# Kernel tuning notes

Hardware: AMD Instinct MI355X
Metric: run time of the kernel (lower is better)

Reference implementation:

```python
import jax, jax.numpy as jnp
import numpy as np

B, S, E = 2, 2048, 1024
H = 16
D = E // H  # 64
SCALE = D ** -0.5


def setup_inputs() -> dict:
    key = jax.random.key(0)
    ks = jax.random.split(key, 9)
    w = lambda k: jax.random.normal(k, (E, E), dtype=jnp.float32) * 0.02
    b = lambda k: jax.random.normal(k, (E,), dtype=jnp.float32) * 0.02
    return {
        "hidden_states": jax.random.normal(ks[0], (B, S, E), dtype=jnp.float32),
        "q_w": w(ks[1]), "q_b": b(ks[2]),
        "k_w": w(ks[3]), "k_b": b(ks[4]),
        "v_w": w(ks[5]), "v_b": b(ks[6]),
        "o_w": w(ks[7]), "o_b": b(ks[8]),
    }


def reference(hidden_states, q_w, q_b, k_w, k_b, v_w, v_b, o_w, o_b):
    dtype = hidden_states.dtype
    # torch Linear: y = x @ W^T + b
    q = hidden_states @ q_w.T + q_b
    k = hidden_states @ k_w.T + k_b
    v = hidden_states @ v_w.T + v_b
    # [B,S,E] -> [B*H, S, D]
    split = lambda t: t.reshape(B, S, H, D).transpose(0, 2, 1, 3).reshape(B * H, S, D)
    q, k, v = split(q), split(k), split(v)
    # upcast_attention: fp32 QK^T, scaled (baddbmm with beta=0, no mask)
    scores = SCALE * jnp.einsum("bqd,bkd->bqk", q.astype(jnp.float32), k.astype(jnp.float32))
    # upcast_softmax: fp32 softmax over last dim (transpose_qk=False), cast back
    probs = jax.nn.softmax(scores, axis=-1).astype(dtype)
    # PV bmm, merge heads, out_proj (dropout p=0.0 -> identity)
    out = jnp.einsum("bqk,bkd->bqd", probs, v)
    out = out.reshape(B, H, S, D).transpose(0, 2, 1, 3).reshape(B, S, E)
    return out @ o_w.T + o_b
```

## Files before the change

### kernel.cpp

```cpp
#include <hip/hip_runtime.h>

typedef __bf16 bf16x8 __attribute__((ext_vector_type(8)));
typedef __bf16 bf16x4 __attribute__((ext_vector_type(4)));
typedef float  f32x4  __attribute__((ext_vector_type(4)));

#define CS 0.18033688011112042f

__device__ __forceinline__ float fast_exp2(float x) {
    return __builtin_amdgcn_exp2f(x);
}

__device__ __forceinline__ f32x4 MFMA(bf16x8 a, bf16x8 b, f32x4 c) {
    return __builtin_amdgcn_mfma_f32_16x16x32_bf16(a, b, c, 0, 0, 0);
}

__global__ __launch_bounds__(256) void cvt5_kernel(
    const float* __restrict__ s0, const float* __restrict__ s1,
    const float* __restrict__ s2, const float* __restrict__ s3,
    const float* __restrict__ s4,
    __bf16* __restrict__ d0, __bf16* __restrict__ d1, __bf16* __restrict__ d2,
    __bf16* __restrict__ d3, __bf16* __restrict__ d4)
{
    int blk = blockIdx.x;
    const float* src; __bf16* dst; int base;
    if (blk < 4096)      { src = s0; dst = d0; base = blk; }
    else if (blk < 5120) { src = s1; dst = d1; base = blk - 4096; }
    else if (blk < 6144) { src = s2; dst = d2; base = blk - 5120; }
    else if (blk < 7168) { src = s3; dst = d3; base = blk - 6144; }
    else                 { src = s4; dst = d4; base = blk - 7168; }
    int i = base * 1024 + threadIdx.x * 4;
    float4 v = *(const float4*)(src + i);
    bf16x4 o;
    o[0] = (__bf16)v.x; o[1] = (__bf16)v.y; o[2] = (__bf16)v.z; o[3] = (__bf16)v.w;
    *(bf16x4*)(dst + i) = o;
}

template <typename OutT, int BN>
__device__ __forceinline__ void gemm_core(const __bf16* __restrict__ A,
                                          const __bf16* __restrict__ W,
                                          const float* __restrict__ bias,
                                          OutT* __restrict__ C,
                                          int m0, int n0, bool vtrans)
{
    constexpr int NJ = BN / 32;
    __shared__ __bf16 As[128 * 64];
    __shared__ __bf16 Bs[BN * 64];

    const int tid  = threadIdx.x;
    const int lane = tid & 63;
    const int w    = tid >> 6;
    const int wm   = w & 1;
    const int wn   = w >> 1;
    const int s    = lane & 15;
    const int q    = lane >> 4;

    f32x4 acc[4][NJ];
#pragma unroll
    for (int i = 0; i < 4; i++)
#pragma unroll
        for (int j = 0; j < NJ; j++)
#pragma unroll
            for (int r = 0; r < 4; r++) acc[i][j][r] = 0.0f;

    bf16x8 apre[4], bpre[NJ];
#pragma unroll
    for (int t = 0; t < 4; t++) {
        int c = tid + 256 * t, row = c >> 3, cc = c & 7;
        apre[t] = *(const bf16x8*)(A + (size_t)(m0 + row) * 1024 + cc * 8);
    }
#pragma unroll
    for (int t = 0; t < NJ; t++) {
        int c = tid + 256 * t, row = c >> 3, cc = c & 7;
        bpre[t] = *(const bf16x8*)(W + (size_t)(n0 + row) * 1024 + cc * 8);
    }

    for (int k0 = 0; k0 < 1024; k0 += 64) {
        __syncthreads();
#pragma unroll
        for (int t = 0; t < 4; t++) {
            int c = tid + 256 * t, row = c >> 3, cc = c & 7;
            *(bf16x8*)&As[row * 64 + ((cc ^ (row & 7)) << 3)] = apre[t];
        }
#pragma unroll
        for (int t = 0; t < NJ; t++) {
            int c = tid + 256 * t, row = c >> 3, cc = c & 7;
            *(bf16x8*)&Bs[row * 64 + ((cc ^ (row & 7)) << 3)] = bpre[t];
        }
        __syncthreads();

        if (k0 < 1024 - 64) {
            int kn = k0 + 64;
#pragma unroll
            for (int t = 0; t < 4; t++) {
                int c = tid + 256 * t, row = c >> 3, cc = c & 7;
                apre[t] = *(const bf16x8*)(A + (size_t)(m0 + row) * 1024 + kn + cc * 8);
            }
#pragma unroll
            for (int t = 0; t < NJ; t++) {
                int c = tid + 256 * t, row = c >> 3, cc = c & 7;
                bpre[t] = *(const bf16x8*)(W + (size_t)(n0 + row) * 1024 + kn + cc * 8);
            }
        }

#pragma unroll
        for (int kk = 0; kk < 2; kk++) {
            bf16x8 af[4], bf[NJ];
#pragma unroll
            for (int i = 0; i < 4; i++) {
                int row = wm * 64 + i * 16 + s;
                int idx = row * 64 + ((((kk << 2) + q) ^ (row & 7)) << 3);
                af[i] = *(const bf16x8*)&As[idx];
            }
#pragma unroll
            for (int j = 0; j < NJ; j++) {
                int row = wn * (BN / 2) + j * 16 + s;
                int idx = row * 64 + ((((kk << 2) + q) ^ (row & 7)) << 3);
                bf[j] = *(const bf16x8*)&Bs[idx];
            }
#pragma unroll
            for (int i = 0; i < 4; i++)
#pragma unroll
                for (int j = 0; j < NJ; j++)
                    acc[i][j] = MFMA(af[i], bf[j], acc[i][j]);
        }
    }

    if (vtrans) {
        __bf16* Vt = (__bf16*)C;
#pragma unroll
        for (int j = 0; j < NJ; j++) {
            int col = n0 + wn * (BN / 2) + j * 16 + s;
            int h   = col >> 6;
            int d   = col & 63;
            float bv = bias[col];
#pragma unroll
            for (int i = 0; i < 4; i++) {
                int rowb = m0 + wm * 64 + i * 16 + q * 4;
                int b    = rowb >> 11;
                int srow = rowb & 2047;
                bf16x4 pk;
#pragma unroll
                for (int r = 0; r < 4; r++) pk[r] = (__bf16)(acc[i][j][r] + bv);
                *(bf16x4*)&Vt[(size_t)((b * 16 + h) * 64 + d) * 2048 + srow] = pk;
            }
        }
    } else {
#pragma unroll
        for (int j = 0; j < NJ; j++) {
            int col = n0 + wn * (BN / 2) + j * 16 + s;
            float bv = bias[col];
#pragma unroll
            for (int i = 0; i < 4; i++) {
                int rowb = m0 + wm * 64 + i * 16 + q * 4;
#pragma unroll
                for (int r = 0; r < 4; r++) {
                    C[(size_t)(rowb + r) * 1024 + col] = (OutT)(acc[i][j][r] + bv);
                }
            }
        }
    }
}

__global__ __launch_bounds__(256) void gemm_qkv_kernel(
    const __bf16* __restrict__ X,
    const __bf16* __restrict__ Wq, const float* __restrict__ bq,
    const __bf16* __restrict__ Wk, const float* __restrict__ bk,
    const __bf16* __restrict__ Wv, const float* __restrict__ bv,
    __bf16* __restrict__ Q, __bf16* __restrict__ K, __bf16* __restrict__ Vt)
{
    int mt   = blockIdx.x & 31;
    int ntot = blockIdx.x >> 5;
    int which = ntot >> 3;
    const __bf16* W    = (which == 0) ? Wq : (which == 1) ? Wk : Wv;
    const float*  bias = (which == 0) ? bq : (which == 1) ? bk : bv;
    __bf16*       Out  = (which == 0) ? Q  : (which == 1) ? K  : Vt;
    gemm_core<__bf16, 128>(X, W, bias, Out, mt * 128, (ntot & 7) * 128, which == 2);
}

__global__ __launch_bounds__(256) void gemm_o_kernel(
    const __bf16* __restrict__ Ain, const __bf16* __restrict__ Wo,
    const float* __restrict__ bo, float* __restrict__ Out)
{
    int mt = blockIdx.x & 31;
    int nt = blockIdx.x >> 5;
    gemm_core<float, 64>(Ain, Wo, bo, Out, mt * 128, nt * 64, false);
}

__global__ __launch_bounds__(256, 2) void attn_kernel(
    const __bf16* __restrict__ Q, const __bf16* __restrict__ K,
    const __bf16* __restrict__ Vt, __bf16* __restrict__ O)
{
    __shared__ __bf16 k_lds[128 * 64];
    __shared__ __bf16 vt_lds[64 * 128];
    __shared__ __bf16 p_lds[4 * 32 * 128];

    const int bh = blockIdx.x >> 4;
    const int qt = blockIdx.x & 15;
    const int b  = bh >> 4;
    const int h  = bh & 15;

    const int tid  = threadIdx.x;
    const int lane = tid & 63;
    const int w    = tid >> 6;
    const int s    = lane & 15;
    const int q    = lane >> 4;

    bf16x8 aq[2][2];
#pragma unroll
    for (int i = 0; i < 2; i++)
#pragma unroll
        for (int kd = 0; kd < 2; kd++) {
            int row = qt * 128 + w * 32 + i * 16 + s;
            aq[i][kd] = *(const bf16x8*)(Q + (size_t)(b * 2048 + row) * 1024 +
                                         h * 64 + kd * 32 + q * 8);
        }

    f32x4 acc_o[2][4];
    float lst[2][4];
#pragma unroll
    for (int i = 0; i < 2; i++)
#pragma unroll
        for (int r = 0; r < 4; r++) {
            lst[i][r] = 0.0f;
#pragma unroll
            for (int jd = 0; jd < 4; jd++) acc_o[i][jd][r] = 0.0f;
        }

    const int pbase = w * 32 * 128;

    bf16x8 kpre[4], vpre[4];
#pragma unroll
    for (int t = 0; t < 4; t++) {
        int c = tid + 256 * t;
        int krow = c >> 3, cc = c & 7;
        kpre[t] = *(const bf16x8*)(K + (size_t)(b * 2048 + krow) * 1024 +
                                   h * 64 + cc * 8);
        int d = c >> 4, ck = c & 15;
        vpre[t] = *(const bf16x8*)(Vt + (size_t)(bh * 64 + d) * 2048 + ck * 8);
    }

    for (int kc = 0; kc < 16; kc++) {
        __syncthreads();
#pragma unroll
        for (int t = 0; t < 4; t++) {
            int c = tid + 256 * t;
            int krow = c >> 3, cc = c & 7;
            int rho  = ((krow & 7) << 4) | (krow >> 3);
            *(bf16x8*)&k_lds[rho * 64 + ((cc ^ (rho & 7)) << 3)] = kpre[t];
            int d = c >> 4, ck = c & 15;
            *(bf16x8*)&vt_lds[(d * 16 + (ck ^ (d & 7))) << 3] = vpre[t];
        }
        __syncthreads();

        int kb2 = ((kc + 1) & 15) * 128;
#pragma unroll
        for (int t = 0; t < 4; t++) {
            int c = tid + 256 * t;
            int krow = c >> 3, cc = c & 7;
            kpre[t] = *(const bf16x8*)(K + (size_t)(b * 2048 + kb2 + krow) * 1024 +
                                       h * 64 + cc * 8);
            int d = c >> 4, ck = c & 15;
            vpre[t] = *(const bf16x8*)(Vt + (size_t)(bh * 64 + d) * 2048 + kb2 + ck * 8);
        }

        f32x4 sc[2][8];
#pragma unroll
        for (int i = 0; i < 2; i++)
#pragma unroll
            for (int j = 0; j < 8; j++)
#pragma unroll
                for (int r = 0; r < 4; r++) sc[i][j][r] = 0.0f;
#pragma unroll
        for (int kd = 0; kd < 2; kd++) {
#pragma unroll
            for (int j = 0; j < 8; j++) {
                int row = j * 16 + s;
                int idx = row * 64 + ((((kd << 2) + q) ^ (row & 7)) << 3);
                bf16x8 bf = *(const bf16x8*)&k_lds[idx];
                sc[0][j] = MFMA(aq[0][kd], bf, sc[0][j]);
                sc[1][j] = MFMA(aq[1][kd], bf, sc[1][j]);
            }
        }

#pragma unroll
        for (int i = 0; i < 2; i++)
#pragma unroll
            for (int r = 0; r < 4; r++) {
                int prow = i * 16 + q * 4 + r;
                bf16x8 pk;
                float rsum = 0.0f;
#pragma unroll
                for (int j = 0; j < 8; j++) {
                    float p = fast_exp2(sc[i][j][r] * CS);
                    rsum += p;
                    pk[j] = (__bf16)p;
                }
                lst[i][r] += rsum;
                int chunkp = s ^ (prow & 15);
                *(bf16x8*)&p_lds[pbase + prow * 128 + (chunkp << 3)] = pk;
            }

#pragma unroll
        for (int kk = 0; kk < 4; kk++) {
            bf16x8 ap[2];
#pragma unroll
            for (int i = 0; i < 2; i++) {
                int prow = i * 16 + s;
                int chunkr = ((kk << 2) + q) ^ s;
                ap[i] = *(const bf16x8*)&p_lds[pbase + prow * 128 + (chunkr << 3)];
            }
#pragma unroll
            for (int jd = 0; jd < 4; jd++) {
                int d    = jd * 16 + s;
                int vidx = (d * 16 + (((kk << 2) + q) ^ (d & 7))) << 3;
                bf16x8 bv = *(const bf16x8*)&vt_lds[vidx];
                acc_o[0][jd] = MFMA(ap[0], bv, acc_o[0][jd]);
                acc_o[1][jd] = MFMA(ap[1], bv, acc_o[1][jd]);
            }
        }
    }

#pragma unroll
    for (int i = 0; i < 2; i++)
#pragma unroll
        for (int r = 0; r < 4; r++) {
#pragma unroll
            for (int off = 1; off < 16; off <<= 1)
                lst[i][r] += __shfl_xor(lst[i][r], off);
        }

#pragma unroll
    for (int i = 0; i < 2; i++)
#pragma unroll
        for (int jd = 0; jd < 4; jd++)
#pragma unroll
            for (int r = 0; r < 4; r++) {
                int row = qt * 128 + w * 32 + i * 16 + q * 4 + r;
                int col = h * 64 + jd * 16 + s;
                float v = acc_o[i][jd][r] / lst[i][r];
                O[(size_t)(b * 2048 + row) * 1024 + col] = (__bf16)v;
            }
}

extern "C" void kernel_launch(void* const* d_in, const int* in_sizes, int n_in,
                              void* d_out, int out_size, void* d_ws, size_t ws_size,
                              hipStream_t stream)
{
    const float* hs = (const float*)d_in[0];
    const float* qw = (const float*)d_in[1];
    const float* qb = (const float*)d_in[2];
    const float* kw = (const float*)d_in[3];
    const float* kb = (const float*)d_in[4];
    const float* vw = (const float*)d_in[5];
    const float* vb = (const float*)d_in[6];
    const float* ow = (const float*)d_in[7];
    const float* ob = (const float*)d_in[8];
    float* out = (float*)d_out;

    char* ws = (char*)d_ws;
    const size_t MB = (size_t)1024 * 1024;
    __bf16* Xb  = (__bf16*)(ws);
    __bf16* Wqb = (__bf16*)(ws +  8 * MB);
    __bf16* Wkb = (__bf16*)(ws + 10 * MB);
    __bf16* Wvb = (__bf16*)(ws + 12 * MB);
    __bf16* Wob = (__bf16*)(ws + 14 * MB);
    __bf16* Qb  = (__bf16*)(ws + 16 * MB);
    __bf16* Kb  = (__bf16*)(ws + 24 * MB);
    __bf16* Vtb = (__bf16*)(ws + 32 * MB);
    __bf16* Ab  = (__bf16*)(ws + 40 * MB);

    cvt5_kernel<<<dim3(8192), dim3(256), 0, stream>>>(hs, qw, kw, vw, ow,
                                                      Xb, Wqb, Wkb, Wvb, Wob);

    gemm_qkv_kernel<<<dim3(768), dim3(256), 0, stream>>>(Xb, Wqb, qb, Wkb, kb, Wvb, vb,
                                                         Qb, Kb, Vtb);
    attn_kernel<<<dim3(512), dim3(256), 0, stream>>>(Qb, Kb, Vtb, Ab);
    gemm_o_kernel<<<dim3(512), dim3(256), 0, stream>>>(Ab, Wob, ob, out);
}
```

Baseline: 189.1 us.

## Rewrite attention with 32x32 MFMA, transposed S, register-resident P via permlane swap

Restructures the attention kernel to use 32x32x16 MFMA with K as the A operand so the score tile comes out transposed. The probabilities are then repacked in registers with v_permlane32_swap and fed straight into the PV MFMA, which removes the P round-trip through LDS. K/V tiles shrink to 64 keys and are double-buffered in LDS, so each iteration needs one barrier instead of two. This raises register pressure with 16-wide accumulators and relies on the gfx950 permlane instruction and on the lane mapping being correct.

```diff
diff --git a/kernel.cpp b/kernel.cpp
--- a/kernel.cpp
+++ b/kernel.cpp
@@ -3,6 +3,8 @@
 typedef __bf16 bf16x8 __attribute__((ext_vector_type(8)));
 typedef __bf16 bf16x4 __attribute__((ext_vector_type(4)));
 typedef float  f32x4  __attribute__((ext_vector_type(4)));
+typedef float  f32x16 __attribute__((ext_vector_type(16)));
+typedef unsigned int u32x4 __attribute__((ext_vector_type(4)));
 
 #define CS 0.18033688011112042f
 
@@ -12,6 +14,19 @@
 
 __device__ __forceinline__ f32x4 MFMA(bf16x8 a, bf16x8 b, f32x4 c) {
     return __builtin_amdgcn_mfma_f32_16x16x32_bf16(a, b, c, 0, 0, 0);
+}
+__device__ __forceinline__ f32x16 MFMA32(bf16x8 a, bf16x8 b, f32x16 c) {
+    return __builtin_amdgcn_mfma_f32_32x32x16_bf16(a, b, c, 0, 0, 0);
+}
+
+__device__ __forceinline__ unsigned pk2(float a, float b) {
+    union { __bf16 h[2]; unsigned u; } x;
+    x.h[0] = (__bf16)a; x.h[1] = (__bf16)b;
+    return x.u;
+}
+
+__device__ __forceinline__ void swap32(unsigned &a, unsigned &b) {
+    asm volatile("v_permlane32_swap_b32 %0, %1" : "+v"(a), "+v"(b));
 }
 
 __global__ __launch_bounds__(256) void cvt5_kernel(
@@ -190,9 +205,8 @@
     const __bf16* __restrict__ Q, const __bf16* __restrict__ K,
     const __bf16* __restrict__ Vt, __bf16* __restrict__ O)
 {
-    __shared__ __bf16 k_lds[128 * 64];
-    __shared__ __bf16 vt_lds[64 * 128];
-    __shared__ __bf16 p_lds[4 * 32 * 128];
+    __shared__ __bf16 k_lds[2][64 * 64];
+    __shared__ __bf16 vt_lds[2][64 * 64];
 
     const int bh = blockIdx.x >> 4;
     const int qt = blockIdx.x & 15;
@@ -202,144 +216,142 @@
     const int tid  = threadIdx.x;
     const int lane = tid & 63;
     const int w    = tid >> 6;
-    const int s    = lane & 15;
-    const int q    = lane >> 4;
-
-    bf16x8 aq[2][2];
-#pragma unroll
-    for (int i = 0; i < 2; i++)
-#pragma unroll
-        for (int kd = 0; kd < 2; kd++) {
-            int row = qt * 128 + w * 32 + i * 16 + s;
-            aq[i][kd] = *(const bf16x8*)(Q + (size_t)(b * 2048 + row) * 1024 +
-                                         h * 64 + kd * 32 + q * 8);
-        }
-
-    f32x4 acc_o[2][4];
-    float lst[2][4];
-#pragma unroll
-    for (int i = 0; i < 2; i++)
-#pragma unroll
-        for (int r = 0; r < 4; r++) {
-            lst[i][r] = 0.0f;
-#pragma unroll
-            for (int jd = 0; jd < 4; jd++) acc_o[i][jd][r] = 0.0f;
-        }
-
-    const int pbase = w * 32 * 128;
-
-    bf16x8 kpre[4], vpre[4];
-#pragma unroll
-    for (int t = 0; t < 4; t++) {
+    const int qc   = lane & 31;
+    const int hi   = lane >> 5;
+
+    bf16x8 bq[4];
+    {
+        const int qrow = qt * 128 + w * 32 + qc;
+        const __bf16* qp = Q + (size_t)(b * 2048 + qrow) * 1024 + h * 64 + hi * 8;
+#pragma unroll
+        for (int kd = 0; kd < 4; kd++)
+            bq[kd] = *(const bf16x8*)(qp + kd * 16);
+    }
+
+    f32x16 acc[2];
+#pragma unroll
+    for (int nb = 0; nb < 2; nb++)
+#pragma unroll
+        for (int r = 0; r < 16; r++) acc[nb][r] = 0.0f;
+    float lst = 0.0f;
+
+    const __bf16* Kbase = K  + (size_t)b * 2048 * 1024 + h * 64;
+    const __bf16* Vbase = Vt + (size_t)bh * 64 * 2048;
+
+    bf16x8 kpre[2], vpre[2];
+#pragma unroll
+    for (int t = 0; t < 2; t++) {
         int c = tid + 256 * t;
-        int krow = c >> 3, cc = c & 7;
-        kpre[t] = *(const bf16x8*)(K + (size_t)(b * 2048 + krow) * 1024 +
-                                   h * 64 + cc * 8);
-        int d = c >> 4, ck = c & 15;
-        vpre[t] = *(const bf16x8*)(Vt + (size_t)(bh * 64 + d) * 2048 + ck * 8);
-    }
-
-    for (int kc = 0; kc < 16; kc++) {
+        int krow = c >> 3, d16 = c & 7;
+        kpre[t] = *(const bf16x8*)(Kbase + (size_t)krow * 1024 + d16 * 8);
+        vpre[t] = *(const bf16x8*)(Vbase + (size_t)krow * 2048 + d16 * 8);
+    }
+#pragma unroll
+    for (int t = 0; t < 2; t++) {
+        int c = tid + 256 * t;
+        int krow = c >> 3, d16 = c & 7;
+        *(bf16x8*)&k_lds[0][krow * 64 + ((d16 ^ (krow & 7)) << 3)] = kpre[t];
+        *(bf16x8*)&vt_lds[0][krow * 64 + ((d16 ^ (krow & 7)) << 3)] = vpre[t];
+    }
+#pragma unroll
+    for (int t = 0; t < 2; t++) {
+        int c = tid + 256 * t;
+        int krow = c >> 3, d16 = c & 7;
+        kpre[t] = *(const bf16x8*)(Kbase + (size_t)(64 + krow) * 1024 + d16 * 8);
+        vpre[t] = *(const bf16x8*)(Vbase + (size_t)krow * 2048 + 64 + d16 * 8);
+    }
+    __syncthreads();
+
+    int cur = 0;
+    for (int kc = 0; kc < 32; kc++) {
+        {
+            __bf16* kwb = k_lds[cur ^ 1];
+            __bf16* vwb = vt_lds[cur ^ 1];
+#pragma unroll
+            for (int t = 0; t < 2; t++) {
+                int c = tid + 256 * t;
+                int krow = c >> 3, d16 = c & 7;
+                kwb[0] ? (void)0 : (void)0;
+                *(bf16x8*)&kwb[krow * 64 + ((d16 ^ (krow & 7)) << 3)] = kpre[t];
+                *(bf16x8*)&vwb[krow * 64 + ((d16 ^ (krow & 7)) << 3)] = vpre[t];
+            }
+        }
+        {
+            int kb2g = ((kc + 2) & 31) * 64;
+#pragma unroll
+            for (int t = 0; t < 2; t++) {
+                int c = tid + 256 * t;
+                int krow = c >> 3, d16 = c & 7;
+                kpre[t] = *(const bf16x8*)(Kbase + (size_t)(kb2g + krow) * 1024 + d16 * 8);
+                vpre[t] = *(const bf16x8*)(Vbase + (size_t)krow * 2048 + kb2g + d16 * 8);
+            }
+        }
+
+        const __bf16* kbuf = k_lds[cur];
+        const __bf16* vbuf = vt_lds[cur];
+
+        f32x16 sc[2];
+#pragma unroll
+        for (int mb = 0; mb < 2; mb++)
+#pragma unroll
+            for (int r = 0; r < 16; r++) sc[mb][r] = 0.0f;
+#pragma unroll
+        for (int mb = 0; mb < 2; mb++) {
+            int row = mb * 32 + qc;
+            int rsw = row & 7;
+#pragma unroll
+            for (int kd = 0; kd < 4; kd++) {
+                bf16x8 af = *(const bf16x8*)&kbuf[row * 64 + ((((kd << 1) | hi) ^ rsw) << 3)];
+                sc[mb] = MFMA32(af, bq[kd], sc[mb]);
+            }
+        }
+
+#pragma unroll
+        for (int mb = 0; mb < 2; mb++) {
+            float e[16];
+            float rs = 0.0f;
+#pragma unroll
+            for (int r = 0; r < 16; r++) {
+                e[r] = fast_exp2(sc[mb][r] * CS);
+                rs += e[r];
+            }
+            lst += rs;
+#pragma unroll
+            for (int bb = 0; bb < 2; bb++) {
+                unsigned w0 = pk2(e[8 * bb + 0], e[8 * bb + 1]);
+                unsigned w1 = pk2(e[8 * bb + 2], e[8 * bb + 3]);
+                unsigned w2 = pk2(e[8 * bb + 4], e[8 * bb + 5]);
+                unsigned w3 = pk2(e[8 * bb + 6], e[8 * bb + 7]);
+                swap32(w0, w2);
+                swap32(w1, w3);
+                u32x4 pw; pw[0] = w0; pw[1] = w1; pw[2] = w2; pw[3] = w3;
+                bf16x8 pa = __builtin_bit_cast(bf16x8, pw);
+                int kslot = ((mb << 1) | bb) << 1;
+#pragma unroll
+                for (int nb = 0; nb < 2; nb++) {
+                    int d = nb * 32 + qc;
+                    bf16x8 bv = *(const bf16x8*)&vbuf[d * 64 + (((kslot | hi) ^ (d & 7)) << 3)];
+                    acc[nb] = MFMA32(pa, bv, acc[nb]);
+                }
+            }
+        }
         __syncthreads();
-#pragma unroll
-        for (int t = 0; t < 4; t++) {
-            int c = tid + 256 * t;
-            int krow = c >> 3, cc = c & 7;
-            int rho  = ((krow & 7) << 4) | (krow >> 3);
-            *(bf16x8*)&k_lds[rho * 64 + ((cc ^ (rho & 7)) << 3)] = kpre[t];
-            int d = c >> 4, ck = c & 15;
-            *(bf16x8*)&vt_lds[(d * 16 + (ck ^ (d & 7))) << 3] = vpre[t];
-        }
-        __syncthreads();
-
-        int kb2 = ((kc + 1) & 15) * 128;
-#pragma unroll
-        for (int t = 0; t < 4; t++) {
-            int c = tid + 256 * t;
-            int krow = c >> 3, cc = c & 7;
-            kpre[t] = *(const bf16x8*)(K + (size_t)(b * 2048 + kb2 + krow) * 1024 +
-                                       h * 64 + cc * 8);
-            int d = c >> 4, ck = c & 15;
-            vpre[t] = *(const bf16x8*)(Vt + (size_t)(bh * 64 + d) * 2048 + kb2 + ck * 8);
-        }
-
-        f32x4 sc[2][8];
-#pragma unroll
-        for (int i = 0; i < 2; i++)
-#pragma unroll
-            for (int j = 0; j < 8; j++)
-#pragma unroll
-                for (int r = 0; r < 4; r++) sc[i][j][r] = 0.0f;
-#pragma unroll
-        for (int kd = 0; kd < 2; kd++) {
-#pragma unroll
-            for (int j = 0; j < 8; j++) {
-                int row = j * 16 + s;
-                int idx = row * 64 + ((((kd << 2) + q) ^ (row & 7)) << 3);
-                bf16x8 bf = *(const bf16x8*)&k_lds[idx];
-                sc[0][j] = MFMA(aq[0][kd], bf, sc[0][j]);
-                sc[1][j] = MFMA(aq[1][kd], bf, sc[1][j]);
-            }
-        }
-
-#pragma unroll
-        for (int i = 0; i < 2; i++)
-#pragma unroll
-            for (int r = 0; r < 4; r++) {
-                int prow = i * 16 + q * 4 + r;
-                bf16x8 pk;
-                float rsum = 0.0f;
-#pragma unroll
-                for (int j = 0; j < 8; j++) {
-                    float p = fast_exp2(sc[i][j][r] * CS);
-                    rsum += p;
-                    pk[j] = (__bf16)p;
-                }
-                lst[i][r] += rsum;
-                int chunkp = s ^ (prow & 15);
-                *(bf16x8*)&p_lds[pbase + prow * 128 + (chunkp << 3)] = pk;
-            }
-
-#pragma unroll
-        for (int kk = 0; kk < 4; kk++) {
-            bf16x8 ap[2];
-#pragma unroll
-            for (int i = 0; i < 2; i++) {
-                int prow = i * 16 + s;
-                int chunkr = ((kk << 2) + q) ^ s;
-                ap[i] = *(const bf16x8*)&p_lds[pbase + prow * 128 + (chunkr << 3)];
-            }
-#pragma unroll
-            for (int jd = 0; jd < 4; jd++) {
-                int d    = jd * 16 + s;
-                int vidx = (d * 16 + (((kk << 2) + q) ^ (d & 7))) << 3;
-                bf16x8 bv = *(const bf16x8*)&vt_lds[vidx];
-                acc_o[0][jd] = MFMA(ap[0], bv, acc_o[0][jd]);
-                acc_o[1][jd] = MFMA(ap[1], bv, acc_o[1][jd]);
-            }
-        }
-    }
-
-#pragma unroll
-    for (int i = 0; i < 2; i++)
-#pragma unroll
-        for (int r = 0; r < 4; r++) {
-#pragma unroll
-            for (int off = 1; off < 16; off <<= 1)
-                lst[i][r] += __shfl_xor(lst[i][r], off);
-        }
-
-#pragma unroll
-    for (int i = 0; i < 2; i++)
-#pragma unroll
-        for (int jd = 0; jd < 4; jd++)
-#pragma unroll
-            for (int r = 0; r < 4; r++) {
-                int row = qt * 128 + w * 32 + i * 16 + q * 4 + r;
-                int col = h * 64 + jd * 16 + s;
-                float v = acc_o[i][jd][r] / lst[i][r];
-                O[(size_t)(b * 2048 + row) * 1024 + col] = (__bf16)v;
-            }
+        cur ^= 1;
+    }
+
+    float lt = lst + __shfl_xor(lst, 32);
+
+    const size_t obase = (size_t)(b * 2048 + qt * 128 + w * 32) * 1024 + h * 64;
+#pragma unroll
+    for (int r = 0; r < 16; r++) {
+        int row_rel = (r & 3) + 8 * (r >> 2) + 4 * hi;
+        float lr = __shfl(lt, row_rel);
+        float inv = 1.0f / lr;
+#pragma unroll
+        for (int nb = 0; nb < 2; nb++) {
+            O[obase + (size_t)row_rel * 1024 + nb * 32 + qc] = (__bf16)(acc[nb][r] * inv);
+        }
+    }
 }
 
 extern "C" void kernel_launch(void* const* d_in, const int* in_sizes, int n_in,
```

After: 187.9 us. Within noise of the previous version (-0.6%).
